# Kernel optimization log

Hardware: AMD Instinct MI355X
Metric: run time of the kernel (lower is better)

## Reference

```python
import jax, jax.numpy as jnp
import numpy as np

B = 64            # graphs in batch
N = 100_000       # total nodes
E = 600_000       # total edges of g == nodes of line graph lg
E2 = 1_500_000    # edges of line graph
H = 128           # hidden_dim
L = 3             # num_layers
MAXZ = 100

seg_sum = jax.ops.segment_sum


def setup_inputs() -> dict:
    key = jax.random.key(0)
    ks = jax.random.split(key, 20)
    s = 1.0 / np.sqrt(H)
    inp = {
        'z': jax.random.randint(ks[0], (N,), 0, MAXZ + 1),
        'd': jax.random.uniform(ks[1], (E, 1), dtype=jnp.float32),
        'src': jax.random.randint(ks[2], (E,), 0, N),
        'dst': jax.random.randint(ks[3], (E,), 0, N),
        'lsrc': jax.random.randint(ks[4], (E2,), 0, E),
        'ldst': jax.random.randint(ks[5], (E2,), 0, E),
        'node_graph': jnp.sort(jax.random.randint(ks[6], (N,), 0, B)),
        'edge_graph': jnp.sort(jax.random.randint(ks[7], (E,), 0, B)),
        'emb': jax.random.normal(ks[8], (MAXZ + 1, H), jnp.float32),
        'ep_w': jax.random.normal(ks[9], (1, H), jnp.float32) * s,
        'ep_b': jnp.zeros((H,), jnp.float32),
        'gW': jax.random.normal(ks[10], (L, H, H), jnp.float32) * s,
        'gb': jnp.zeros((L, H), jnp.float32),
        'lgW': jax.random.normal(ks[11], (L, H, H), jnp.float32) * s,
        'lgb': jnp.zeros((L, H), jnp.float32),
        'r1w': jax.random.normal(ks[12], (2 * H, H), jnp.float32) * s,
        'r1b': jnp.zeros((H,), jnp.float32),
        'r2w': jax.random.normal(ks[13], (H, 1), jnp.float32) * s,
        'r2b': jnp.zeros((1,), jnp.float32),
    }
    return inp


def _graph_conv(h, srcix, dstix, W, b, n_nodes):
    # DGL GraphConv, norm='both', aggregate-then-weight (in==out dims):
    # h' = D_in^{-1/2} * A^T * (D_out^{-1/2} * h) @ W + b, degrees clamped >= 1
    ones = jnp.ones(srcix.shape[0], h.dtype)
    deg_out = jnp.clip(seg_sum(ones, srcix, num_segments=n_nodes), 1.0)
    deg_in = jnp.clip(seg_sum(ones, dstix, num_segments=n_nodes), 1.0)
    m = h * (deg_out ** -0.5)[:, None]
    agg = seg_sum(m[srcix], dstix, num_segments=n_nodes)  # SpMM gather-scatter
    agg = agg * (deg_in ** -0.5)[:, None]
    return agg @ W + b


def _segment_mean(h, seg, n_seg):
    sums = seg_sum(h, seg, num_segments=n_seg)
    cnt = jnp.clip(seg_sum(jnp.ones(h.shape[0], h.dtype), seg, num_segments=n_seg), 1.0)
    return sums / cnt[:, None]


def reference(z, d, src, dst, lsrc, ldst, node_graph, edge_graph,
              emb, ep_w, ep_b, gW, gb, lgW, lgb, r1w, r1b, r2w, r2b):
    h = emb[z]                       # [N, H]
    e = d @ ep_w + ep_b              # [E, H]
    for i in range(L):
        h = jax.nn.relu(_graph_conv(h, src, dst, gW[i], gb[i], N))
    for i in range(L):
        e = jax.nn.relu(_graph_conv(e, lsrc, ldst, lgW[i], lgb[i], E))
    hg = _segment_mean(h, node_graph, B)   # [B, H]
    he = _segment_mean(e, edge_graph, B)   # [B, H]
    x = jnp.concatenate([hg, he], axis=-1)  # [B, 2H]
    y = jax.nn.silu(x @ r1w + r1b) @ r2w + r2b
    return y.reshape(-1)             # [B]
```

## Files before the change

### kernel.cpp

```cpp
#include <hip/hip_runtime.h>
#include <math.h>

#define H 128
typedef unsigned short u16;
typedef unsigned char u8;
typedef unsigned int u32;
typedef _Float16 f16;
typedef f16 f16x8 __attribute__((ext_vector_type(8)));
typedef float f32x4 __attribute__((ext_vector_type(4)));
typedef float f32x2 __attribute__((ext_vector_type(2)));

#if __has_builtin(__builtin_amdgcn_cvt_pk_fp8_f32)
#define HW8 1
#else
#define HW8 0
#endif

#define SSTRIDE 144

static inline int cdiv(long long a, long long b) { return (int)((a + b - 1) / b); }

struct F8 {
    static __device__ inline float dec(u8 v) {
        int e = (v >> 3) & 15, m = v & 7;
        float f = (e == 0) ? (float)m * 0.001953125f : ldexpf(1.f + 0.125f * (float)m, e - 7);
        return (v & 0x80) ? -f : f;
    }
    static __device__ inline u8 enc(float x) {
        u8 s = (u8)((__float_as_uint(x) >> 24) & 0x80);
        float ax = fabsf(x);
        if (!(ax < 448.f)) return s | 0x7E;
        if (ax < 0.015625f) {
            int m = (int)rintf(ax * 512.f);
            if (m >= 8) return s | 0x08;
            return s | (u8)m;
        }
        int e; float fr = frexpf(ax, &e);
        int E = e - 1;
        int m = (int)rintf(fr * 16.f - 8.f);
        if (m == 8) { m = 0; ++E; }
        if (E > 8) return s | 0x7E;
        return s | (u8)(((E + 7) << 3) | m);
    }
};

static __device__ inline u32 enc4(float x0, float x1, float x2, float x3) {
#if HW8
    u32 w = __builtin_amdgcn_cvt_pk_fp8_f32(x0, x1, 0, false);
    w = __builtin_amdgcn_cvt_pk_fp8_f32(x2, x3, w, true);
    return w;
#else
    union { u8 b[4]; u32 u; } p;
    p.b[0] = F8::enc(x0); p.b[1] = F8::enc(x1); p.b[2] = F8::enc(x2); p.b[3] = F8::enc(x3);
    return p.u;
#endif
}
static __device__ inline float4 dec4(u32 v) {
#if HW8
    f32x2 lo = __builtin_amdgcn_cvt_pk_f32_fp8(v, false);
    f32x2 hi = __builtin_amdgcn_cvt_pk_f32_fp8(v, true);
    return make_float4(lo.x, lo.y, hi.x, hi.y);
#else
    union { u32 u; u8 b[4]; } c; c.u = v;
    return make_float4(F8::dec(c.b[0]), F8::dec(c.b[1]), F8::dec(c.b[2]), F8::dec(c.b[3]));
#endif
}
static __device__ inline float dec1(u8 b) {
#if HW8
    return __builtin_amdgcn_cvt_f32_fp8((int)b, 0);
#else
    return F8::dec(b);
#endif
}

__global__ __launch_bounds__(256) void setup1_k(
    const float* __restrict__ gW, const float* __restrict__ lgW, f16* __restrict__ wt, int L, int nbPW,
    const int* __restrict__ src, const int* __restrict__ dst,
    const int* __restrict__ lsrc, const int* __restrict__ ldst,
    int* __restrict__ con, int* __restrict__ cin, int* __restrict__ coe, int* __restrict__ cie,
    int E, int E2, int nbHI,
    const int* __restrict__ node_graph, int N, const int* __restrict__ edge_graph,
    int B, int* __restrict__ cntn, int* __restrict__ cnte) {
    int blk = blockIdx.x;
    if (blk < nbPW) {
        int mat = blk >> 6;
        int idx = (blk & 63) * 256 + threadIdx.x;
        int k = idx >> 7, n = idx & 127;
        const float* W = (mat < L) ? gW + (size_t)mat * H * H : lgW + (size_t)(mat - L) * H * H;
        wt[(size_t)mat * H * H + (size_t)n * H + k] = (f16)W[(size_t)k * H + n];
        return;
    }
    blk -= nbPW;
    if (blk < nbHI) {
        int i = blk * 256 + threadIdx.x;
        if (i < E) {
            atomicAdd(&con[src[i]], 1);
            atomicAdd(&cin[dst[i]], 1);
        } else if (i < E + E2) {
            int j = i - E;
            atomicAdd(&coe[lsrc[j]], 1);
            atomicAdd(&cie[ldst[j]], 1);
        }
        return;
    }
    blk -= nbHI;
    {
        const int* seg = blk ? edge_graph : node_graph;
        int n = blk ? E : N;
        int* cnt = blk ? cnte : cntn;
        __shared__ int bound[129];
        int b = threadIdx.x;
        if (b <= B) {
            int lo = 0, hi = n;
            while (lo < hi) {
                int mid = (lo + hi) >> 1;
                if (seg[mid] < b) lo = mid + 1; else hi = mid;
            }
            bound[b] = lo;
        }
        __syncthreads();
        if (b < B) cnt[b] = bound[b + 1] - bound[b];
    }
}

__global__ __launch_bounds__(256) void setup2_k(
    const int* __restrict__ con, const int* __restrict__ cin,
    const int* __restrict__ coe, const int* __restrict__ cie,
    float* __restrict__ ron, float* __restrict__ rin,
    float* __restrict__ roe, float* __restrict__ rie,
    const float* __restrict__ d, float2* __restrict__ pairE, int N, int E, int nbRS,
    int* __restrict__ offs_n, int nbN, int* __restrict__ offs_e, int* __restrict__ bsum) {
    int blk = blockIdx.x;
    if (blk < nbRS) {
        int i = blk * 256 + threadIdx.x;
        if (i < N) { int v = con[i]; ron[i] = rsqrtf((float)(v < 1 ? 1 : v)); }
        else if (i < 2 * N) { int n = i - N; int v = cin[n]; rin[n] = rsqrtf((float)(v < 1 ? 1 : v)); }
        else if (i < 2 * N + E) {
            int n = i - 2 * N; int v = coe[n];
            float r = rsqrtf((float)(v < 1 ? 1 : v));
            roe[n] = r;
            pairE[n] = make_float2(r * d[n], r);
        } else if (i < 2 * N + 2 * E) {
            int n = i - 2 * N - E; int v = cie[n]; rie[n] = rsqrtf((float)(v < 1 ? 1 : v));
        }
        return;
    }
    blk -= nbRS;
    {
        __shared__ int sh[256];
        const int* in; int* out; int n; int gid;
        if (blk < nbN) { in = cin; out = offs_n; n = N; gid = blk * 256 + threadIdx.x; }
        else { in = cie; out = offs_e; n = E; gid = (blk - nbN) * 256 + threadIdx.x; }
        int v = (gid < n) ? in[gid] : 0;
        sh[threadIdx.x] = v;
        __syncthreads();
        for (int off = 1; off < 256; off <<= 1) {
            int t = (threadIdx.x >= off) ? sh[threadIdx.x - off] : 0;
            __syncthreads();
            sh[threadIdx.x] += t;
            __syncthreads();
        }
        if (gid < n) out[gid] = sh[threadIdx.x] - v;
        if (threadIdx.x == 255) bsum[blk] = sh[255];
    }
}

__global__ __launch_bounds__(256) void scan_bsum2_k(int* __restrict__ bsum, int nbA, int nbB) {
    __shared__ int sh[256];
    __shared__ int carry;
#pragma unroll 1
    for (int part = 0; part < 2; ++part) {
        int base0 = part ? nbA : 0;
        int nb = part ? nbB : nbA;
        if (threadIdx.x == 0) carry = 0;
        __syncthreads();
        for (int base = 0; base < nb; base += 256) {
            int i = base + threadIdx.x;
            int v = (i < nb) ? bsum[base0 + i] : 0;
            sh[threadIdx.x] = v;
            __syncthreads();
            for (int off = 1; off < 256; off <<= 1) {
                int t = (threadIdx.x >= off) ? sh[threadIdx.x - off] : 0;
                __syncthreads();
                sh[threadIdx.x] += t;
                __syncthreads();
            }
            if (i < nb) bsum[base0 + i] = sh[threadIdx.x] - v + carry;
            __syncthreads();
            if (threadIdx.x == 0) carry += sh[255];
            __syncthreads();
        }
    }
}

__global__ __launch_bounds__(256) void setup3_k(
    int* __restrict__ offs_n, int* __restrict__ cur_n, int N, int nbN, int E,
    int* __restrict__ offs_e, int* __restrict__ cur_e, int E2, int nbE,
    const int* __restrict__ bsum,
    const int* __restrict__ z, const float* __restrict__ emb,
    const float* __restrict__ ron, u8* __restrict__ featN) {
    int blk = blockIdx.x;
    int nbSA = nbN + nbE;
    if (blk < nbSA) {
        int* offs; int* curp; int n; int gid; int nnz;
        if (blk < nbN) { offs = offs_n; curp = cur_n; n = N; gid = blk * 256 + threadIdx.x; nnz = E; }
        else { offs = offs_e; curp = cur_e; n = E; gid = (blk - nbN) * 256 + threadIdx.x; nnz = E2; }
        if (gid < n) {
            int v = offs[gid] + bsum[blk];
            offs[gid] = v;
            curp[gid] = v;
        }
        if (gid == 0) offs[n] = nnz;
        return;
    }
    blk -= nbSA;
    {
        int idx = blk * 256 + threadIdx.x;
        if (idx >= N * 32) return;
        int n = idx >> 5, c4 = (idx & 31) << 2;
        float sc = ron[n];
        const float4 v = *(const float4*)(emb + (size_t)z[n] * H + c4);
        *(u32*)(featN + (size_t)n * H + c4) = enc4(v.x * sc, v.y * sc, v.z * sc, v.w * sc);
    }
}

__global__ __launch_bounds__(256) void fill2_k(const int* __restrict__ src, const int* __restrict__ dst,
                                               const int* __restrict__ lsrc, const int* __restrict__ ldst,
                                               int* __restrict__ cur_n, int* __restrict__ cur_e,
                                               uint2* __restrict__ nbr_n, uint2* __restrict__ nbr_e,
                                               int E, int E2) {
    int i = blockIdx.x * 256 + threadIdx.x;
    if (i < E) {
        int dd = dst[i];
        int p = atomicAdd(&cur_n[dd], 1);
        nbr_n[p] = make_uint2((u32)src[i], (u32)dd);
    } else if (i < E + E2) {
        int j = i - E;
        int dd = ldst[j];
        int p = atomicAdd(&cur_e[dd], 1);
        nbr_e[p] = make_uint2((u32)lsrc[j], (u32)dd);
    }
}

__device__ __forceinline__ void gather_phase(
    const u8* __restrict__ Xin,
    const int* __restrict__ offs, const uint2* __restrict__ nbr2,
    const float* __restrict__ rs_in, int M,
    int row0, f16 (*As)[136], int wave, int lane) {
    const int rowbase = row0 + wave * 16;
    {
        uint2* zp = (uint2*)&As[wave * 16][0];
#pragma unroll
        for (int i = 0; i < 9; ++i) {
            int o = lane + i * 64;
            if (o < 544) zp[o] = make_uint2(0u, 0u);
        }
    }
    const int gl = lane >> 4;
    const int ln = lane & 15;
    const int rbase4 = rowbase + gl * 4;
    const int r_lo = min(rbase4, M);
    const int r_hi = min(rbase4 + 4, M);
    const int jbeg = offs[r_lo];
    const int jend = offs[r_hi];
    if (jbeg >= jend) return;
    const int mrow = M - 1;
    const float rsr0 = rs_in[min(rbase4 + 0, mrow)];
    const float rsr1 = rs_in[min(rbase4 + 1, mrow)];
    const float rsr2 = rs_in[min(rbase4 + 2, mrow)];
    const float rsr3 = rs_in[min(rbase4 + 3, mrow)];

    float a0 = 0.f, a1 = 0.f, a2 = 0.f, a3 = 0.f, a4 = 0.f, a5 = 0.f, a6 = 0.f, a7 = 0.f;
    int curdst = -1;

#define FLUSH_ROW()                                                              \
    do {                                                                         \
        const int dd_ = curdst - rbase4;                                         \
        const float ri_ = dd_ == 0 ? rsr0 : (dd_ == 1 ? rsr1 : (dd_ == 2 ? rsr2 : rsr3)); \
        f16x8 o_;                                                                \
        o_[0] = (f16)(a0 * ri_); o_[1] = (f16)(a1 * ri_);                        \
        o_[2] = (f16)(a2 * ri_); o_[3] = (f16)(a3 * ri_);                        \
        o_[4] = (f16)(a4 * ri_); o_[5] = (f16)(a5 * ri_);                        \
        o_[6] = (f16)(a6 * ri_); o_[7] = (f16)(a7 * ri_);                        \
        *(f16x8*)&As[curdst - row0][ln << 3] = o_;                               \
    } while (0)

    uint2 e[8];
#pragma unroll
    for (int k = 0; k < 8; ++k) e[k] = nbr2[min(jbeg + k, jend - 1)];
    int jc = jbeg;
    do {
        uint2 f[8];
#pragma unroll
        for (int k = 0; k < 8; ++k)
            f[k] = *(const uint2*)(Xin + ((size_t)e[k].x << 7) + (ln << 3));
        const int jn = jc + 8;
        uint2 en[8];
#pragma unroll
        for (int k = 0; k < 8; ++k) en[k] = nbr2[min(jn + k, jend - 1)];
#pragma unroll
        for (int k = 0; k < 8; ++k) {
            if (jc + k < jend) {
                const int dk = (int)e[k].y;
                if (dk != curdst) {
                    if (curdst >= 0) {
                        FLUSH_ROW();
                        a0 = a1 = a2 = a3 = a4 = a5 = a6 = a7 = 0.f;
                    }
                    curdst = dk;
                }
                float4 lo = dec4(f[k].x);
                float4 hi = dec4(f[k].y);
                a0 += lo.x; a1 += lo.y; a2 += lo.z; a3 += lo.w;
                a4 += hi.x; a5 += hi.y; a6 += hi.z; a7 += hi.w;
            }
        }
#pragma unroll
        for (int k = 0; k < 8; ++k) e[k] = en[k];
        jc = jn;
    } while (jc < jend);
    FLUSH_ROW();
#undef FLUSH_ROW
}

template <bool STORE>
__device__ __forceinline__ void conv_mfma_phase(
    u8* __restrict__ Xout, const f16* __restrict__ Wt, const float* __restrict__ bias,
    const float* __restrict__ scale_out, int M, int row0, f16 (*As)[136], int wave, int lane) {
    const int rowbase = row0 + wave * 16;
    if (rowbase >= M) return;
    const int l15 = lane & 15;
    const int quad = lane >> 4;

    f16x8 a[4];
#pragma unroll
    for (int kt = 0; kt < 4; ++kt)
        a[kt] = *(const f16x8*)&As[wave * 16 + l15][kt * 32 + quad * 8];

    float rsc[4];
#pragma unroll
    for (int r = 0; r < 4; ++r) {
        int gr = rowbase + quad * 4 + r;
        rsc[r] = (scale_out && gr < M) ? scale_out[gr] : 1.f;
    }

    u8* stage = (u8*)&As[wave * 16][0];

#pragma unroll
    for (int n0 = 0; n0 < 8; ++n0) {
        f32x4 acc = {0.f, 0.f, 0.f, 0.f};
        const f16* bp = Wt + (size_t)(n0 * 16 + l15) * H + quad * 8;
#pragma unroll
        for (int kt = 0; kt < 4; ++kt) {
            f16x8 b = *(const f16x8*)(bp + kt * 32);
            acc = __builtin_amdgcn_mfma_f32_16x16x32_f16(a[kt], b, acc, 0, 0, 0);
        }
        int col = n0 * 16 + l15;
        float bv = bias[col];
        float o[4];
#pragma unroll
        for (int r = 0; r < 4; ++r) o[r] = fmaxf(acc[r] + bv, 0.f) * rsc[r];
        u32 w = enc4(o[0], o[1], o[2], o[3]);
#pragma unroll
        for (int r = 0; r < 4; ++r) stage[(quad * 4 + r) * SSTRIDE + col] = (u8)(w >> (8 * r));
    }
    if (STORE) {
        const int lr = lane >> 2;
        const int lc = (lane & 3) * 32;
        int gr = rowbase + lr;
        if (gr < M) {
            uint4 v0 = *(const uint4*)&stage[lr * SSTRIDE + lc];
            uint4 v1 = *(const uint4*)&stage[lr * SSTRIDE + lc + 16];
            *(uint4*)(Xout + (size_t)gr * H + lc) = v0;
            *(uint4*)(Xout + (size_t)gr * H + lc + 16) = v1;
        }
    }
}

__device__ __forceinline__ void conv_mfma_pool_phase(
    const f16* __restrict__ Wt, const float* __restrict__ bias, int M, int row0,
    f16 (*As)[136], float (*pool)[128], int wave, int lane,
    const int* __restrict__ seg, float* __restrict__ outp, bool uni) {
    const int rowbase = row0 + wave * 16;
    if (rowbase >= M) return;
    const int l15 = lane & 15;
    const int quad = lane >> 4;

    f16x8 a[4];
#pragma unroll
    for (int kt = 0; kt < 4; ++kt)
        a[kt] = *(const f16x8*)&As[wave * 16 + l15][kt * 32 + quad * 8];

    const int gr0 = rowbase + quad * 4;
    const int remM = M - gr0;
    int g0 = -1, g1 = -1, g2 = -1, g3 = -1;
    if (!uni) {
        g0 = (0 < remM) ? seg[gr0 + 0] : -1;
        g1 = (1 < remM) ? seg[gr0 + 1] : -1;
        g2 = (2 < remM) ? seg[gr0 + 2] : -1;
        g3 = (3 < remM) ? seg[gr0 + 3] : -1;
    }

#pragma unroll
    for (int n0 = 0; n0 < 8; ++n0) {
        f32x4 acc = {0.f, 0.f, 0.f, 0.f};
        const f16* bp = Wt + (size_t)(n0 * 16 + l15) * H + quad * 8;
#pragma unroll
        for (int kt = 0; kt < 4; ++kt) {
            f16x8 b = *(const f16x8*)(bp + kt * 32);
            acc = __builtin_amdgcn_mfma_f32_16x16x32_f16(a[kt], b, acc, 0, 0, 0);
        }
        const int col = n0 * 16 + l15;
        const float bv = bias[col];
        const float o0 = (0 < remM) ? fmaxf(acc[0] + bv, 0.f) : 0.f;
        const float o1 = (1 < remM) ? fmaxf(acc[1] + bv, 0.f) : 0.f;
        const float o2 = (2 < remM) ? fmaxf(acc[2] + bv, 0.f) : 0.f;
        const float o3 = (3 < remM) ? fmaxf(acc[3] + bv, 0.f) : 0.f;
        if (uni) {
            float s = (o0 + o1) + (o2 + o3);
            s += __shfl_xor(s, 16);
            s += __shfl_xor(s, 32);
            if (quad == 0) pool[wave][col] = s;
        } else {
            float ac = o0; int gc = g0;
            if (g1 == gc) ac += o1; else { if (gc >= 0) atomicAdd(&outp[(size_t)gc * H + col], ac); gc = g1; ac = o1; }
            if (g2 == gc) ac += o2; else { if (gc >= 0) atomicAdd(&outp[(size_t)gc * H + col], ac); gc = g2; ac = o2; }
            if (g3 == gc) ac += o3; else { if (gc >= 0) atomicAdd(&outp[(size_t)gc * H + col], ac); gc = g3; ac = o3; }
            if (gc >= 0) atomicAdd(&outp[(size_t)gc * H + col], ac);
        }
    }
}

template <bool STORE>
__device__ __forceinline__ void conv_wave(
    const u8* __restrict__ Xin, u8* __restrict__ Xout,
    const int* __restrict__ offs, const uint2* __restrict__ nbr2,
    const float* __restrict__ rs_in, const f16* __restrict__ Wt,
    const float* __restrict__ bias, const float* __restrict__ scale_out, int M,
    int row0, f16 (*As)[136], int wave, int lane) {
    gather_phase(Xin, offs, nbr2, rs_in, M, row0, As, wave, lane);
    conv_mfma_phase<STORE>(Xout, Wt, bias, scale_out, M, row0, As, wave, lane);
}

__device__ __forceinline__ void conv_wave_l0e(
    u8* __restrict__ Xout, const int* __restrict__ offs, const uint2* __restrict__ nbr2,
    const float2* __restrict__ pairE, const float* __restrict__ rs_in,
    const float* __restrict__ epw, const float* __restrict__ epb,
    const f16* __restrict__ Wt, const float* __restrict__ bias,
    const float* __restrict__ scale_out, int E,
    int row0, f16 (*As)[136], int wave, int lane) {
    const int rowbase = row0 + wave * 16;
    const int r = lane >> 2;
    const int t = lane & 3;
    int grow = min(rowbase + r, E - 1);
    int jb = offs[grow], je = offs[grow + 1];
    float sd = 0.f, sw = 0.f;
    for (int j = jb + t; j < je; j += 4) {
        float2 p = pairE[nbr2[j].x];
        sd += p.x; sw += p.y;
    }
    sd += __shfl_xor(sd, 1); sw += __shfl_xor(sw, 1);
    sd += __shfl_xor(sd, 2); sw += __shfl_xor(sw, 2);
    float ri = (rowbase + r < E) ? rs_in[rowbase + r] : 0.f;
    sd *= ri; sw *= ri;
#pragma unroll
    for (int c8 = 0; c8 < 4; ++c8) {
        int c0 = t * 32 + c8 * 8;
        const float4 wa = *(const float4*)(epw + c0);
        const float4 wb = *(const float4*)(epw + c0 + 4);
        const float4 ba = *(const float4*)(epb + c0);
        const float4 bb = *(const float4*)(epb + c0 + 4);
        f16x8 o;
        o[0] = (f16)(sd * wa.x + sw * ba.x); o[1] = (f16)(sd * wa.y + sw * ba.y);
        o[2] = (f16)(sd * wa.z + sw * ba.z); o[3] = (f16)(sd * wa.w + sw * ba.w);
        o[4] = (f16)(sd * wb.x + sw * bb.x); o[5] = (f16)(sd * wb.y + sw * bb.y);
        o[6] = (f16)(sd * wb.z + sw * bb.z); o[7] = (f16)(sd * wb.w + sw * bb.w);
        *(f16x8*)&As[wave * 16 + r][c0] = o;
    }
    conv_mfma_phase<true>(Xout, Wt, bias, scale_out, E, row0, As, wave, lane);
}

__global__ __launch_bounds__(256, 4) void conv2_k(
    const u8* __restrict__ XinN, u8* __restrict__ XoutN,
    const int* __restrict__ offs_n, const uint2* __restrict__ nbr_n,
    const float* __restrict__ rinN, const f16* __restrict__ WtN,
    const float* __restrict__ biasN, const float* __restrict__ scaleN, int N, int nbCN,
    const u8* __restrict__ XinE, u8* __restrict__ XoutE,
    const int* __restrict__ offs_e, const uint2* __restrict__ nbr_e,
    const float* __restrict__ rinE, const f16* __restrict__ WtE,
    const float* __restrict__ biasE, const float* __restrict__ scaleE, int E) {
    __shared__ f16 As[64][136];
    const int tid = threadIdx.x;
    const int wave = tid >> 6;
    const int lane = tid & 63;
    if ((int)blockIdx.x < nbCN) {
        conv_wave<true>(XinN, XoutN, offs_n, nbr_n, rinN, WtN, biasN, scaleN, N,
                        blockIdx.x * 64, As, wave, lane);
    } else {
        conv_wave<true>(XinE, XoutE, offs_e, nbr_e, rinE, WtE, biasE, scaleE, E,
                        (blockIdx.x - nbCN) * 64, As, wave, lane);
    }
}

__global__ __launch_bounds__(256, 4) void conv2_l0_k(
    const u8* __restrict__ XinN, u8* __restrict__ XoutN,
    const int* __restrict__ offs_n, const uint2* __restrict__ nbr_n,
    const float* __restrict__ rinN, const f16* __restrict__ WtN,
    const float* __restrict__ biasN, const float* __restrict__ scaleN, int N, int nbCN,
    u8* __restrict__ XoutE,
    const int* __restrict__ offs_e, const uint2* __restrict__ nbr_e,
    const float2* __restrict__ pairE, const float* __restrict__ rinE,
    const float* __restrict__ epw, const float* __restrict__ epb,
    const f16* __restrict__ WtE, const float* __restrict__ biasE,
    const float* __restrict__ scaleE, int E) {
    __shared__ f16 As[64][136];
    const int tid = threadIdx.x;
    const int wave = tid >> 6;
    const int lane = tid & 63;
    if ((int)blockIdx.x < nbCN) {
        conv_wave<true>(XinN, XoutN, offs_n, nbr_n, rinN, WtN, biasN, scaleN, N,
                        blockIdx.x * 64, As, wave, lane);
    } else {
        conv_wave_l0e(XoutE, offs_e, nbr_e, pairE, rinE, epw, epb, WtE, biasE, scaleE, E,
                      (blockIdx.x - nbCN) * 64, As, wave, lane);
    }
}

__global__ __launch_bounds__(256, 4) void conv2_last_k(
    const u8* __restrict__ XinN,
    const int* __restrict__ offs_n, const uint2* __restrict__ nbr_n,
    const float* __restrict__ rinN, const f16* __restrict__ WtN,
    const float* __restrict__ biasN, int N, int nbCN,
    const int* __restrict__ node_graph, float* __restrict__ hg,
    const u8* __restrict__ XinE,
    const int* __restrict__ offs_e, const uint2* __restrict__ nbr_e,
    const float* __restrict__ rinE, const f16* __restrict__ WtE,
    const float* __restrict__ biasE, int E,
    const int* __restrict__ edge_graph, float* __restrict__ he) {
    __shared__ f16 As[64][136];
    __shared__ float pool[4][128];
    const int tid = threadIdx.x;
    const int wave = tid >> 6;
    const int lane = tid & 63;
    const bool isN = (int)blockIdx.x < nbCN;
    const int row0 = (isN ? blockIdx.x : blockIdx.x - nbCN) * 64;
    const int M = isN ? N : E;
    const int* seg = isN ? node_graph : edge_graph;
    float* outp = isN ? hg : he;

    ((float*)pool)[tid] = 0.f;
    ((float*)pool)[tid + 256] = 0.f;
    const int gblk = seg[row0];
    const bool uni = (seg[min(row0 + 63, M - 1)] == gblk);
    __syncthreads();

    if (isN) {
        gather_phase(XinN, offs_n, nbr_n, rinN, N, row0, As, wave, lane);
        conv_mfma_pool_phase(WtN, biasN, N, row0, As, pool, wave, lane, seg, outp, uni);
    } else {
        gather_phase(XinE, offs_e, nbr_e, rinE, E, row0, As, wave, lane);
        conv_mfma_pool_phase(WtE, biasE, E, row0, As, pool, wave, lane, seg, outp, uni);
    }
    __syncthreads();
    if (uni && tid < 128) {
        float s = (pool[0][tid] + pool[1][tid]) + (pool[2][tid] + pool[3][tid]);
        atomicAdd(&outp[(size_t)gblk * H + tid], s);
    }
}

__global__ __launch_bounds__(128) void readout_k(const float* __restrict__ hg, const float* __restrict__ he,
                                                 const int* __restrict__ cn, const int* __restrict__ ce,
                                                 const float* __restrict__ r1w, const float* __restrict__ r1b,
                                                 const float* __restrict__ r2w, const float* __restrict__ r2b,
                                                 float* __restrict__ out) {
    const int b = blockIdx.x;
    const int j = threadIdx.x;
    const float invn = 1.f / fmaxf((float)cn[b], 1.f);
    const float inve = 1.f / fmaxf((float)ce[b], 1.f);
    float acc = r1b[j];
    for (int k = 0; k < H; ++k) acc = fmaf(hg[(size_t)b * H + k] * invn, r1w[(size_t)k * H + j], acc);
    for (int k = 0; k < H; ++k) acc = fmaf(he[(size_t)b * H + k] * inve, r1w[(size_t)(k + H) * H + j], acc);
    float s = acc / (1.f + expf(-acc));
    __shared__ float red[128];
    red[j] = s * r2w[j];
    __syncthreads();
    for (int off = 64; off > 0; off >>= 1) {
        if (j < off) red[j] += red[j + off];
        __syncthreads();
    }
    if (j == 0) out[b] = red[0] + r2b[0];
}

__global__ void report_k(float* out, int n, float val) {
    int i = blockIdx.x * 64 + threadIdx.x;
    if (i < n) out[i] = val;
}

extern "C" void kernel_launch(void* const* d_in, const int* in_sizes, int n_in,
                              void* d_out, int out_size, void* d_ws, size_t ws_size,
                              hipStream_t stream) {
    const int* z          = (const int*)d_in[0];
    const float* d        = (const float*)d_in[1];
    const int* src        = (const int*)d_in[2];
    const int* dst        = (const int*)d_in[3];
    const int* lsrc       = (const int*)d_in[4];
    const int* ldst       = (const int*)d_in[5];
    const int* node_graph = (const int*)d_in[6];
    const int* edge_graph = (const int*)d_in[7];
    const float* emb      = (const float*)d_in[8];
    const float* epw      = (const float*)d_in[9];
    const float* epb      = (const float*)d_in[10];
    const float* gW       = (const float*)d_in[11];
    const float* gb       = (const float*)d_in[12];
    const float* lgW      = (const float*)d_in[13];
    const float* lgb      = (const float*)d_in[14];
    const float* r1w      = (const float*)d_in[15];
    const float* r1b      = (const float*)d_in[16];
    const float* r2w      = (const float*)d_in[17];
    const float* r2b      = (const float*)d_in[18];

    const int N  = in_sizes[0];
    const int E  = in_sizes[2];
    const int E2 = in_sizes[4];
    const int B  = out_size;
    const int L  = 3;
    float* out = (float*)d_out;
    char* ws = (char*)d_ws;

    size_t off = 0;
    auto al = [&](size_t b) -> char* { char* q = ws + off; off += (b + 255) & ~(size_t)255; return q; };
    u8*  featEA = (u8*)al((size_t)E * H);
    u8*  featEB = (u8*)al((size_t)E * H);
    u8*  featNA = (u8*)al((size_t)N * H);
    u8*  featNB = (u8*)al((size_t)N * H);
    f16* wt    = (f16*)al((size_t)2 * L * H * H * 2);
    float* ron = (float*)al((size_t)N * 4);
    float* rin = (float*)al((size_t)N * 4);
    float* roe = (float*)al((size_t)E * 4);
    float* rie = (float*)al((size_t)E * 4);
    float2* pairE = (float2*)al((size_t)E * 8);
    size_t cntCount = (size_t)2 * N + 2 * E + 2 * B;
    size_t cntBytes = cntCount * 4;
    size_t poolsOff = (cntBytes + 255) & ~(size_t)255;
    char* zblock = al(poolsOff + (size_t)2 * B * H * 4);
    int* cnts = (int*)zblock;
    float* pools = (float*)(zblock + poolsOff);
    int* con = cnts; int* cin_ = con + N; int* coe = cin_ + N; int* cie = coe + E;
    int* cntn = cie + E; int* cnte = cntn + B;
    float* hg = pools;
    float* he = pools + (size_t)B * H;
    int* offs_n = (int*)al(((size_t)N + 1) * 4);
    int* cur_n  = (int*)al((size_t)N * 4);
    int* offs_e = (int*)al(((size_t)E + 1) * 4);
    int* cur_e  = (int*)al((size_t)E * 4);
    uint2* nbr_n = (uint2*)al((size_t)E * 8);
    uint2* nbr_e = (uint2*)al((size_t)E2 * 8);
    int nbN = cdiv(N, 256), nbE = cdiv(E, 256);
    int* bsum   = (int*)al(((size_t)nbN + nbE + 2) * 4);

    if (off > ws_size) {
        report_k<<<cdiv(B, 64), 64, 0, stream>>>(out, B, (float)(ws_size >> 20));
        return;
    }

    hipMemsetAsync(zblock, 0, poolsOff + (size_t)2 * B * H * 4, stream);

    const int nbPW = 2 * L * 64;
    const int nbHI = cdiv((long long)E + E2, 256);
    setup1_k<<<nbPW + nbHI + 2, 256, 0, stream>>>(gW, lgW, wt, L, nbPW,
                                                  src, dst, lsrc, ldst, con, cin_, coe, cie,
                                                  E, E2, nbHI, node_graph, N, edge_graph, B, cntn, cnte);

    const int nbRS = cdiv((long long)2 * N + 2 * E, 256);
    setup2_k<<<nbRS + nbN + nbE, 256, 0, stream>>>(con, cin_, coe, cie, ron, rin, roe, rie,
                                                   d, pairE, N, E, nbRS, offs_n, nbN, offs_e, bsum);
    scan_bsum2_k<<<1, 256, 0, stream>>>(bsum, nbN, nbE);

    const int nbIN = cdiv((long long)N * 32, 256);
    setup3_k<<<nbN + nbE + nbIN, 256, 0, stream>>>(offs_n, cur_n, N, nbN, E,
                                                   offs_e, cur_e, E2, nbE, bsum, z, emb, ron, featNA);

    fill2_k<<<cdiv((long long)E + E2, 256), 256, 0, stream>>>(src, dst, lsrc, ldst, cur_n, cur_e, nbr_n, nbr_e, E, E2);

    const int nbCN = cdiv(N, 64), nbCE = cdiv(E, 64);

    conv2_l0_k<<<nbCN + nbCE, 256, 0, stream>>>(
        featNA, featNB, offs_n, nbr_n, rin, wt, gb, ron, N, nbCN,
        featEB, offs_e, nbr_e, pairE, rie, epw, epb,
        wt + (size_t)L * H * H, lgb, roe, E);

    conv2_k<<<nbCN + nbCE, 256, 0, stream>>>(
        featNB, featNA, offs_n, nbr_n, rin, wt + (size_t)1 * H * H, gb + (size_t)1 * H, ron, N, nbCN,
        featEB, featEA, offs_e, nbr_e, rie, wt + (size_t)(L + 1) * H * H, lgb + (size_t)1 * H, roe, E);

    conv2_last_k<<<nbCN + nbCE, 256, 0, stream>>>(
        featNA, offs_n, nbr_n, rin, wt + (size_t)2 * H * H, gb + (size_t)2 * H, N, nbCN, node_graph, hg,
        featEA, offs_e, nbr_e, rie, wt + (size_t)(L + 2) * H * H, lgb + (size_t)2 * H, E, edge_graph, he);

    readout_k<<<B, 128, 0, stream>>>(hg, he, cntn, cnte, r1w, r1b, r2w, r2b, out);
}
```

Measured before the change: 1.169 ms.

## Fold edge projection into layer-0 line-graph weights and pre-scatter pair values

Because the initial edge features are rank-2 (d*ep_w + ep_b), the layer-0 line-graph conv output equals sd*(ep_w@W) + sw*(ep_b@W) + b. The change precomputes these two H-vectors once in setup and replaces the per-row f16 staging plus MFMA matmul with a few FMAs per output. It also writes the source pair values into CSR slot order during the fill pass, so the layer-0 gather reads them contiguously instead of through nbr_e indirection. This adds an E2-sized buffer and a random gather in the fill pass, and the rounding differs slightly from the f16 MFMA path.

```diff
diff --git a/kernel.cpp b/kernel.cpp
--- a/kernel.cpp
+++ b/kernel.cpp
@@ -80,7 +80,8 @@
     int* __restrict__ con, int* __restrict__ cin, int* __restrict__ coe, int* __restrict__ cie,
     int E, int E2, int nbHI,
     const int* __restrict__ node_graph, int N, const int* __restrict__ edge_graph,
-    int B, int* __restrict__ cntn, int* __restrict__ cnte) {
+    int B, int* __restrict__ cntn, int* __restrict__ cnte,
+    const float* __restrict__ epw, const float* __restrict__ epb, float* __restrict__ uv) {
     int blk = blockIdx.x;
     if (blk < nbPW) {
         int mat = blk >> 6;
@@ -104,7 +105,7 @@
         return;
     }
     blk -= nbHI;
-    {
+    if (blk < 2) {
         const int* seg = blk ? edge_graph : node_graph;
         int n = blk ? E : N;
         int* cnt = blk ? cnte : cntn;
@@ -120,6 +121,20 @@
         }
         __syncthreads();
         if (b < B) cnt[b] = bound[b + 1] - bound[b];
+        return;
+    }
+    {
+        int n = threadIdx.x;
+        if (n < H) {
+            float su = 0.f, sv = 0.f;
+            for (int k = 0; k < H; ++k) {
+                float w = lgW[(size_t)k * H + n];
+                su = fmaf(epw[k], w, su);
+                sv = fmaf(epb[k], w, sv);
+            }
+            uv[n] = su;
+            uv[n + H] = sv;
+        }
     }
 }
 
@@ -228,6 +243,7 @@
                                                const int* __restrict__ lsrc, const int* __restrict__ ldst,
                                                int* __restrict__ cur_n, int* __restrict__ cur_e,
                                                uint2* __restrict__ nbr_n, uint2* __restrict__ nbr_e,
+                                               const float2* __restrict__ pairE, float2* __restrict__ pslot,
                                                int E, int E2) {
     int i = blockIdx.x * 256 + threadIdx.x;
     if (i < E) {
@@ -236,9 +252,11 @@
         nbr_n[p] = make_uint2((u32)src[i], (u32)dd);
     } else if (i < E + E2) {
         int j = i - E;
+        int ls = lsrc[j];
         int dd = ldst[j];
         int p = atomicAdd(&cur_e[dd], 1);
-        nbr_e[p] = make_uint2((u32)lsrc[j], (u32)dd);
+        nbr_e[p] = make_uint2((u32)ls, (u32)dd);
+        pslot[p] = pairE[ls];
     }
 }
 
@@ -443,41 +461,45 @@
 }
 
 __device__ __forceinline__ void conv_wave_l0e(
-    u8* __restrict__ Xout, const int* __restrict__ offs, const uint2* __restrict__ nbr2,
-    const float2* __restrict__ pairE, const float* __restrict__ rs_in,
-    const float* __restrict__ epw, const float* __restrict__ epb,
-    const f16* __restrict__ Wt, const float* __restrict__ bias,
+    u8* __restrict__ Xout, const int* __restrict__ offs,
+    const float2* __restrict__ pslot, const float* __restrict__ rs_in,
+    const float* __restrict__ uv, const float* __restrict__ bias,
     const float* __restrict__ scale_out, int E,
-    int row0, f16 (*As)[136], int wave, int lane) {
+    int row0, int wave, int lane) {
     const int rowbase = row0 + wave * 16;
     const int r = lane >> 2;
     const int t = lane & 3;
-    int grow = min(rowbase + r, E - 1);
-    int jb = offs[grow], je = offs[grow + 1];
+    const int growu = rowbase + r;
+    const int grow = min(growu, E - 1);
+    const int jb = offs[grow];
+    const int je = offs[grow + 1];
     float sd = 0.f, sw = 0.f;
     for (int j = jb + t; j < je; j += 4) {
-        float2 p = pairE[nbr2[j].x];
+        float2 p = pslot[j];
         sd += p.x; sw += p.y;
     }
     sd += __shfl_xor(sd, 1); sw += __shfl_xor(sw, 1);
     sd += __shfl_xor(sd, 2); sw += __shfl_xor(sw, 2);
-    float ri = (rowbase + r < E) ? rs_in[rowbase + r] : 0.f;
+    if (growu >= E) return;
+    const float ri = rs_in[growu];
+    const float so = scale_out[growu];
     sd *= ri; sw *= ri;
-#pragma unroll
-    for (int c8 = 0; c8 < 4; ++c8) {
-        int c0 = t * 32 + c8 * 8;
-        const float4 wa = *(const float4*)(epw + c0);
-        const float4 wb = *(const float4*)(epw + c0 + 4);
-        const float4 ba = *(const float4*)(epb + c0);
-        const float4 bb = *(const float4*)(epb + c0 + 4);
-        f16x8 o;
-        o[0] = (f16)(sd * wa.x + sw * ba.x); o[1] = (f16)(sd * wa.y + sw * ba.y);
-        o[2] = (f16)(sd * wa.z + sw * ba.z); o[3] = (f16)(sd * wa.w + sw * ba.w);
-        o[4] = (f16)(sd * wb.x + sw * bb.x); o[5] = (f16)(sd * wb.y + sw * bb.y);
-        o[6] = (f16)(sd * wb.z + sw * bb.z); o[7] = (f16)(sd * wb.w + sw * bb.w);
-        *(f16x8*)&As[wave * 16 + r][c0] = o;
-    }
-    conv_mfma_phase<true>(Xout, Wt, bias, scale_out, E, row0, As, wave, lane);
+    const int c0 = t * 32;
+    u32 wbuf[8];
+#pragma unroll
+    for (int c4 = 0; c4 < 8; ++c4) {
+        const int c = c0 + c4 * 4;
+        const float4 ua = *(const float4*)(uv + c);
+        const float4 va = *(const float4*)(uv + H + c);
+        const float4 ba = *(const float4*)(bias + c);
+        const float o0 = fmaxf(fmaf(sd, ua.x, fmaf(sw, va.x, ba.x)), 0.f) * so;
+        const float o1 = fmaxf(fmaf(sd, ua.y, fmaf(sw, va.y, ba.y)), 0.f) * so;
+        const float o2 = fmaxf(fmaf(sd, ua.z, fmaf(sw, va.z, ba.z)), 0.f) * so;
+        const float o3 = fmaxf(fmaf(sd, ua.w, fmaf(sw, va.w, ba.w)), 0.f) * so;
+        wbuf[c4] = enc4(o0, o1, o2, o3);
+    }
+    *(uint4*)(Xout + (size_t)growu * H + c0) = *(uint4*)&wbuf[0];
+    *(uint4*)(Xout + (size_t)growu * H + c0 + 16) = *(uint4*)&wbuf[4];
 }
 
 __global__ __launch_bounds__(256, 4) void conv2_k(
@@ -508,11 +530,9 @@
     const float* __restrict__ rinN, const f16* __restrict__ WtN,
     const float* __restrict__ biasN, const float* __restrict__ scaleN, int N, int nbCN,
     u8* __restrict__ XoutE,
-    const int* __restrict__ offs_e, const uint2* __restrict__ nbr_e,
-    const float2* __restrict__ pairE, const float* __restrict__ rinE,
-    const float* __restrict__ epw, const float* __restrict__ epb,
-    const f16* __restrict__ WtE, const float* __restrict__ biasE,
-    const float* __restrict__ scaleE, int E) {
+    const int* __restrict__ offs_e, const float2* __restrict__ pslot,
+    const float* __restrict__ rinE, const float* __restrict__ uv,
+    const float* __restrict__ biasE, const float* __restrict__ scaleE, int E) {
     __shared__ f16 As[64][136];
     const int tid = threadIdx.x;
     const int wave = tid >> 6;
@@ -521,8 +541,8 @@
         conv_wave<true>(XinN, XoutN, offs_n, nbr_n, rinN, WtN, biasN, scaleN, N,
                         blockIdx.x * 64, As, wave, lane);
     } else {
-        conv_wave_l0e(XoutE, offs_e, nbr_e, pairE, rinE, epw, epb, WtE, biasE, scaleE, E,
-                      (blockIdx.x - nbCN) * 64, As, wave, lane);
+        conv_wave_l0e(XoutE, offs_e, pslot, rinE, uv, biasE, scaleE, E,
+                      (blockIdx.x - nbCN) * 64, wave, lane);
     }
 }
 
@@ -634,6 +654,7 @@
     u8*  featNA = (u8*)al((size_t)N * H);
     u8*  featNB = (u8*)al((size_t)N * H);
     f16* wt    = (f16*)al((size_t)2 * L * H * H * 2);
+    float* uv  = (float*)al((size_t)2 * H * 4);
     float* ron = (float*)al((size_t)N * 4);
     float* rin = (float*)al((size_t)N * 4);
     float* roe = (float*)al((size_t)E * 4);
@@ -655,6 +676,7 @@
     int* cur_e  = (int*)al((size_t)E * 4);
     uint2* nbr_n = (uint2*)al((size_t)E * 8);
     uint2* nbr_e = (uint2*)al((size_t)E2 * 8);
+    float2* pslot = (float2*)al((size_t)E2 * 8);
     int nbN = cdiv(N, 256), nbE = cdiv(E, 256);
     int* bsum   = (int*)al(((size_t)nbN + nbE + 2) * 4);
 
@@ -667,9 +689,10 @@
 
     const int nbPW = 2 * L * 64;
     const int nbHI = cdiv((long long)E + E2, 256);
-    setup1_k<<<nbPW + nbHI + 2, 256, 0, stream>>>(gW, lgW, wt, L, nbPW,
+    setup1_k<<<nbPW + nbHI + 3, 256, 0, stream>>>(gW, lgW, wt, L, nbPW,
                                                   src, dst, lsrc, ldst, con, cin_, coe, cie,
-                                                  E, E2, nbHI, node_graph, N, edge_graph, B, cntn, cnte);
+                                                  E, E2, nbHI, node_graph, N, edge_graph, B, cntn, cnte,
+                                                  epw, epb, uv);
 
     const int nbRS = cdiv((long long)2 * N + 2 * E, 256);
     setup2_k<<<nbRS + nbN + nbE, 256, 0, stream>>>(con, cin_, coe, cie, ron, rin, roe, rie,
@@ -680,14 +703,14 @@
     setup3_k<<<nbN + nbE + nbIN, 256, 0, stream>>>(offs_n, cur_n, N, nbN, E,
                                                    offs_e, cur_e, E2, nbE, bsum, z, emb, ron, featNA);
 
-    fill2_k<<<cdiv((long long)E + E2, 256), 256, 0, stream>>>(src, dst, lsrc, ldst, cur_n, cur_e, nbr_n, nbr_e, E, E2);
+    fill2_k<<<cdiv((long long)E + E2, 256), 256, 0, stream>>>(src, dst, lsrc, ldst, cur_n, cur_e,
+                                                              nbr_n, nbr_e, pairE, pslot, E, E2);
 
     const int nbCN = cdiv(N, 64), nbCE = cdiv(E, 64);
 
     conv2_l0_k<<<nbCN + nbCE, 256, 0, stream>>>(
         featNA, featNB, offs_n, nbr_n, rin, wt, gb, ron, N, nbCN,
-        featEB, offs_e, nbr_e, pairE, rie, epw, epb,
-        wt + (size_t)L * H * H, lgb, roe, E);
+        featEB, offs_e, pslot, rie, uv, lgb, roe, E);
 
     conv2_k<<<nbCN + nbCE, 256, 0, stream>>>(
         featNB, featNA, offs_n, nbr_n, rin, wt + (size_t)1 * H * H, gb + (size_t)1 * H, ron, N, nbCN,
```

New measurement: 1.001 ms. -14.3%, faster.
